# Optimization experiments

Hardware: AMD Instinct MI355X
Metric: run time of the kernel (lower is better)

Reference implementation:

```python
import jax, jax.numpy as jnp
import numpy as np

B, S, HID = 2, 2048, 2048
NH, NKV, D = 16, 4, 128  # heads, kv heads, dim_per_head
ROPE_BASE = 10000.0


def setup_inputs() -> dict:
    key = jax.random.key(0)
    ks = jax.random.split(key, 5)
    x = jax.random.normal(ks[0], (B, S, HID), jnp.float32)
    wq = jax.random.normal(ks[1], (HID, NH * D), jnp.float32) * 0.02
    wk = jax.random.normal(ks[2], (HID, NKV * D), jnp.float32) * 0.02
    wv = jax.random.normal(ks[3], (HID, NKV * D), jnp.float32) * 0.02
    wo = jax.random.normal(ks[4], (NH * D, HID), jnp.float32) * 0.02
    inv_freq = 1.0 / (ROPE_BASE ** (jnp.arange(0, D, 2, dtype=jnp.float32) / D))
    freqs = jnp.outer(jnp.arange(S, dtype=jnp.float32), inv_freq)  # [S, D/2]
    cos, sin = jnp.cos(freqs), jnp.sin(freqs)
    mask = jnp.tril(jnp.ones((S, S), dtype=bool))  # causal, True = attend
    return {"x": x, "wq": wq, "wk": wk, "wv": wv, "wo": wo,
            "cos": cos, "sin": sin, "mask": mask}


def _rope_interleave(t, cos, sin):
    # t: [B, H, S, D]; cos/sin: [S, D/2]; interleaved pairs (even, odd)
    te, to = t[..., ::2], t[..., 1::2]
    c, s = cos[None, None], sin[None, None]
    re = te * c - to * s
    ro = to * c + te * s
    return jnp.stack([re, ro], axis=-1).reshape(t.shape)


def reference(x, wq, wk, wv, wo, cos, sin, mask):
    b, s, _ = x.shape
    # QKV projections + shape(): [B, S, hid] -> [B, H, S, D]
    q = (x @ wq).reshape(b, s, NH, D).transpose(0, 2, 1, 3)
    k = (x @ wk).reshape(b, s, NKV, D).transpose(0, 2, 1, 3)
    v = (x @ wv).reshape(b, s, NKV, D).transpose(0, 2, 1, 3)
    q = _rope_interleave(q, cos, sin)
    k = _rope_interleave(k, cos, sin)
    # GQA: repeat each kv head heads//heads_kv times consecutively
    rep = NH // NKV
    k = jnp.repeat(k, rep, axis=1)
    v = jnp.repeat(v, rep, axis=1)
    scores = jnp.einsum('bhqd,bhkd->bhqk', q, k) * (D ** -0.5)
    scores = scores.astype(jnp.float32)
    scores = jnp.where(mask[None, None], scores, jnp.finfo(jnp.float32).min)
    attn = jax.nn.softmax(scores, axis=-1).astype(x.dtype)
    ctx = jnp.einsum('bhqk,bhkd->bhqd', attn, v)
    ctx = ctx.transpose(0, 2, 1, 3).reshape(b, s, NH * D)  # unshape()
    return ctx @ wo
```

## Files before the change

kernel.cpp:

```cpp
#include <hip/hip_runtime.h>
#include <hip/hip_bf16.h>
#include <math.h>

#define S_LEN 2048
#define HIDW 2048
#define NHEAD 16
#define NKVH 4
#define HD 128
#define NB 2
#define MROWS (NB * S_LEN)
#define QKVN (NHEAD * HD + 2 * NKVH * HD)
#define KOFF (NHEAD * HD)
#define VOFF (NHEAD * HD + NKVH * HD)

typedef __bf16 bf16_t;
typedef __bf16 bf16x4_t __attribute__((ext_vector_type(4)));
typedef __bf16 bf16x8_t __attribute__((ext_vector_type(8)));
typedef float f32x4_t __attribute__((ext_vector_type(4)));

__device__ __forceinline__ void gload_lds16(const bf16_t* g, bf16_t* l) {
  __builtin_amdgcn_global_load_lds(
      (const __attribute__((address_space(1))) void*)g,
      (__attribute__((address_space(3))) void*)l, 16, 0, 0);
}

__device__ __forceinline__ f32x4_t zero4() {
  f32x4_t z = {0.f, 0.f, 0.f, 0.f};
  return z;
}

__device__ __forceinline__ float fexp2(float x) {
#if __has_builtin(__builtin_amdgcn_exp2f)
  return __builtin_amdgcn_exp2f(x);
#else
  return exp2f(x);
#endif
}

__global__ __launch_bounds__(256) void k_cvt8(const float* __restrict__ in,
                                              bf16_t* __restrict__ out, int n8) {
  int i = blockIdx.x * 256 + threadIdx.x;
  if (i >= n8) return;
  const float4* p = (const float4*)(in + (size_t)i * 8);
  float4 a = p[0], b = p[1];
  bf16x8_t r;
  r[0] = (bf16_t)a.x; r[1] = (bf16_t)a.y; r[2] = (bf16_t)a.z; r[3] = (bf16_t)a.w;
  r[4] = (bf16_t)b.x; r[5] = (bf16_t)b.y; r[6] = (bf16_t)b.z; r[7] = (bf16_t)b.w;
  *(bf16x8_t*)(out + (size_t)i * 8) = r;
}

__global__ __launch_bounds__(256) void k_tr_cvt(const float* __restrict__ in,
                                                bf16_t* __restrict__ out, int R, int C) {
  __shared__ float t[32][33];
  int c0 = blockIdx.x * 32, r0 = blockIdx.y * 32;
  int tx = threadIdx.x & 31, ty = threadIdx.x >> 5;
#pragma unroll
  for (int rr = ty; rr < 32; rr += 8) t[rr][tx] = in[(size_t)(r0 + rr) * C + c0 + tx];
  __syncthreads();
#pragma unroll
  for (int rr = ty; rr < 32; rr += 8)
    out[(size_t)(c0 + rr) * R + r0 + tx] = (bf16_t)t[tx][rr];
}

template <int EPI, int BMH>
__global__ __launch_bounds__(512, 2) void k_gemm256(const bf16_t* __restrict__ A,
                                                    const bf16_t* __restrict__ Bt,
                                                    void* __restrict__ Cout,
                                                    int M, int N, int K, int nby,
                                                    const float* __restrict__ cosT,
                                                    const float* __restrict__ sinT) {
  __shared__ bf16_t As[2][BMH * 128 * 64];
  __shared__ bf16_t Bs[2][256 * 64];

  int tid = threadIdx.x;
  int lane = tid & 63, wid = tid >> 6;
  int l15 = lane & 15, lg = lane >> 4;
  int wrb = (wid >> 2) * (BMH * 64);
  int wcb = (wid & 3) * 64;

  int nwg = gridDim.x;
  int qx = nwg >> 3;
  int lin = blockIdx.x;
  int wg = (lin & 7) * qx + (lin >> 3);
  int row0 = (wg / nby) * (BMH * 128), col0 = (wg % nby) * 256;

  int srow = tid >> 3;
  int scol = ((tid & 7) ^ (srow & 7)) * 8;
  const bf16_t* Ag = A + (size_t)(row0 + srow) * K + scol;
  const bf16_t* Bg = Bt + (size_t)(col0 + srow) * K + scol;

  f32x4_t acc[BMH * 4][4];
#pragma unroll
  for (int i = 0; i < BMH * 4; i++)
#pragma unroll
    for (int j = 0; j < 4; j++) acc[i][j] = zero4();

  int xr = (l15 & 7) << 4;
  int nk = K >> 6;

  auto stA = [&](int tt, int u) {
    gload_lds16(Ag + (size_t)u * 64 * K + (size_t)tt * 64,
                As[tt & 1] + u * 4096 + tid * 8);
  };
  auto stB = [&](int tt, int u) {
    gload_lds16(Bg + (size_t)u * 64 * K + (size_t)tt * 64,
                Bs[tt & 1] + u * 4096 + tid * 8);
  };

  for (int tt = 0; tt < 2 && tt < nk; tt++) {
    for (int u = 0; u < BMH * 2; u++) stA(tt, u);
    for (int u = 0; u < 4; u++) stB(tt, u);
  }
  if (nk > 1) {
    if constexpr (BMH == 2) asm volatile("s_waitcnt vmcnt(8)" ::: "memory");
    else asm volatile("s_waitcnt vmcnt(6)" ::: "memory");
  } else {
    asm volatile("s_waitcnt vmcnt(0)" ::: "memory");
  }
  __builtin_amdgcn_s_barrier();
  __builtin_amdgcn_sched_barrier(0);

  for (int t = 0; t < nk; t++) {
    int cur = t & 1;
    const char* Ac = (const char*)As[cur];
    const char* Bc = (const char*)Bs[cur];
    bool pf = (t + 2 < nk);

    bf16x8_t af0[4][2], bfr[4][2];
#pragma unroll
    for (int i = 0; i < 4; i++) {
      int row = wrb + i * 16 + l15;
#pragma unroll
      for (int kk = 0; kk < 2; kk++)
        af0[i][kk] = *(const bf16x8_t*)(Ac + ((row * 128 + kk * 64 + lg * 16) ^ xr));
    }
#pragma unroll
    for (int jn = 0; jn < 4; jn++) {
      int rowb = wcb + jn * 16 + l15;
#pragma unroll
      for (int kk = 0; kk < 2; kk++)
        bfr[jn][kk] = *(const bf16x8_t*)(Bc + ((rowb * 128 + kk * 64 + lg * 16) ^ xr));
    }
    __builtin_amdgcn_s_barrier();
    __builtin_amdgcn_s_setprio(1);
    if constexpr (BMH == 2) {
#pragma unroll
      for (int i = 0; i < 4; i++)
#pragma unroll
        for (int j = 0; j < 2; j++)
#pragma unroll
          for (int kk = 0; kk < 2; kk++)
            acc[i][j] = __builtin_amdgcn_mfma_f32_16x16x32_bf16(af0[i][kk], bfr[j][kk],
                                                                acc[i][j], 0, 0, 0);
    } else {
#pragma unroll
      for (int i = 0; i < 4; i++)
#pragma unroll
        for (int kk = 0; kk < 2; kk++)
          acc[i][0] = __builtin_amdgcn_mfma_f32_16x16x32_bf16(af0[i][kk], bfr[0][kk],
                                                              acc[i][0], 0, 0, 0);
    }
    __builtin_amdgcn_s_setprio(0);

    if (pf) {
      stA(t + 2, 0);
      if constexpr (BMH == 2) stA(t + 2, 2);
      else stA(t + 2, 1);
    }
    __builtin_amdgcn_s_barrier();
    __builtin_amdgcn_s_setprio(1);
    if constexpr (BMH == 2) {
#pragma unroll
      for (int i = 0; i < 4; i++)
#pragma unroll
        for (int j = 0; j < 2; j++)
#pragma unroll
          for (int kk = 0; kk < 2; kk++)
            acc[i][2 + j] = __builtin_amdgcn_mfma_f32_16x16x32_bf16(
                af0[i][kk], bfr[2 + j][kk], acc[i][2 + j], 0, 0, 0);
    } else {
#pragma unroll
      for (int i = 0; i < 4; i++)
#pragma unroll
        for (int kk = 0; kk < 2; kk++)
          acc[i][1] = __builtin_amdgcn_mfma_f32_16x16x32_bf16(af0[i][kk], bfr[1][kk],
                                                              acc[i][1], 0, 0, 0);
    }
    __builtin_amdgcn_s_setprio(0);

    bf16x8_t af1[4][2];
    if constexpr (BMH == 2) {
#pragma unroll
      for (int i = 0; i < 4; i++) {
        int row = wrb + 64 + i * 16 + l15;
#pragma unroll
        for (int kk = 0; kk < 2; kk++)
          af1[i][kk] = *(const bf16x8_t*)(Ac + ((row * 128 + kk * 64 + lg * 16) ^ xr));
      }
    }
    if (pf) { stB(t + 2, 0); stB(t + 2, 1); }
    __builtin_amdgcn_s_barrier();
    __builtin_amdgcn_s_setprio(1);
    if constexpr (BMH == 2) {
#pragma unroll
      for (int i = 0; i < 4; i++)
#pragma unroll
        for (int j = 0; j < 2; j++)
#pragma unroll
          for (int kk = 0; kk < 2; kk++)
            acc[4 + i][j] = __builtin_amdgcn_mfma_f32_16x16x32_bf16(
                af1[i][kk], bfr[j][kk], acc[4 + i][j], 0, 0, 0);
    } else {
#pragma unroll
      for (int i = 0; i < 4; i++)
#pragma unroll
        for (int kk = 0; kk < 2; kk++)
          acc[i][2] = __builtin_amdgcn_mfma_f32_16x16x32_bf16(af0[i][kk], bfr[2][kk],
                                                              acc[i][2], 0, 0, 0);
    }
    __builtin_amdgcn_s_setprio(0);

    if (pf) {
      stB(t + 2, 2); stB(t + 2, 3);
      if constexpr (BMH == 2) { stA(t + 2, 1); stA(t + 2, 3); }
    }
    __builtin_amdgcn_s_barrier();
    __builtin_amdgcn_s_setprio(1);
    if constexpr (BMH == 2) {
#pragma unroll
      for (int i = 0; i < 4; i++)
#pragma unroll
        for (int j = 0; j < 2; j++)
#pragma unroll
          for (int kk = 0; kk < 2; kk++)
            acc[4 + i][2 + j] = __builtin_amdgcn_mfma_f32_16x16x32_bf16(
                af1[i][kk], bfr[2 + j][kk], acc[4 + i][2 + j], 0, 0, 0);
    } else {
#pragma unroll
      for (int i = 0; i < 4; i++)
#pragma unroll
        for (int kk = 0; kk < 2; kk++)
          acc[i][3] = __builtin_amdgcn_mfma_f32_16x16x32_bf16(af0[i][kk], bfr[3][kk],
                                                              acc[i][3], 0, 0, 0);
    }
    __builtin_amdgcn_s_setprio(0);

    if (t + 1 < nk) {
      if (pf) {
        if constexpr (BMH == 2) asm volatile("s_waitcnt vmcnt(8)" ::: "memory");
        else asm volatile("s_waitcnt vmcnt(6)" ::: "memory");
      } else {
        asm volatile("s_waitcnt vmcnt(0)" ::: "memory");
      }
    }
    __builtin_amdgcn_s_barrier();
    __builtin_amdgcn_sched_barrier(0);
  }

  if (EPI == 2) {
    if (col0 < VOFF) {
      int sbase = row0 & (S_LEN - 1);
      bf16_t* cosL = &As[0][0];
      bf16_t* sinL = &Bs[0][0];
#pragma unroll
      for (int k = 0; k < 8; k++) {
        gload_lds16((const bf16_t*)(cosT + (size_t)sbase * 64 + k * 2048 + tid * 4),
                    cosL + k * 4096 + tid * 8);
        gload_lds16((const bf16_t*)(sinT + (size_t)sbase * 64 + k * 2048 + tid * 4),
                    sinL + k * 4096 + tid * 8);
      }
      asm volatile("s_waitcnt vmcnt(0)" ::: "memory");
      __builtin_amdgcn_s_barrier();
      const float* cosF = (const float*)cosL;
      const float* sinF = (const float*)sinL;
      const float QS = 0.08838834764831845f * 1.4426950408889634f;
#pragma unroll
      for (int i = 0; i < BMH * 4; i++) {
#pragma unroll
        for (int j = 0; j < 4; j++) {
          int c = col0 + wcb + j * 16 + l15;
          int rlb = wrb + i * 16 + lg * 4;
          float scale = (c < KOFF) ? QS : 1.0f;
          int p0 = (c & 127) >> 1;
          int codd = c & 1;
#pragma unroll
          for (int qd = 0; qd < 4; qd++) {
            int rl = rlb + qd;
            float self = acc[i][j][qd];
            float other = __shfl_xor(self, 1);
            float cv = cosF[rl * 64 + p0], sv = sinF[rl * 64 + p0];
            float outv = codd ? (self * cv + other * sv) : (self * cv - other * sv);
            ((bf16_t*)Cout)[(size_t)(row0 + rl) * N + c] = (bf16_t)(outv * scale);
          }
        }
      }
    } else {
#pragma unroll
      for (int i = 0; i < BMH * 4; i++) {
#pragma unroll
        for (int j = 0; j < 4; j++) {
          int r = row0 + wrb + i * 16 + lg * 4;
          int c = col0 + wcb + j * 16 + l15;
#pragma unroll
          for (int qd = 0; qd < 4; qd++)
            ((bf16_t*)Cout)[(size_t)(r + qd) * N + c] = (bf16_t)acc[i][j][qd];
        }
      }
    }
  } else {
#pragma unroll
    for (int i = 0; i < BMH * 4; i++) {
#pragma unroll
      for (int j = 0; j < 4; j++) {
        int r = row0 + wrb + i * 16 + lg * 4;
        int c = col0 + wcb + j * 16 + l15;
#pragma unroll
        for (int qd = 0; qd < 4; qd++)
          ((float*)Cout)[(size_t)(r + qd) * N + c] = acc[i][j][qd];
      }
    }
  }
}

__global__ __launch_bounds__(256) void k_vt(const bf16_t* __restrict__ qkv,
                                            bf16_t* __restrict__ vt) {
  __shared__ bf16_t t[32][33];
  int s0 = blockIdx.x * 32;
  int dt = (blockIdx.y & 3) * 32;
  int h = blockIdx.y >> 2;
  int b = blockIdx.z;
  int tx = threadIdx.x & 31, ty = threadIdx.x >> 5;
#pragma unroll
  for (int rr = ty; rr < 32; rr += 8)
    t[rr][tx] = qkv[(size_t)(b * S_LEN + s0 + rr) * QKVN + VOFF + h * HD + dt + tx];
  __syncthreads();
#pragma unroll
  for (int rr = ty; rr < 32; rr += 8)
    vt[((size_t)((b * NKVH + h) * HD + dt + rr)) * S_LEN + s0 + tx] = t[tx][rr];
}

__global__ __launch_bounds__(256, 2) void k_attn(const bf16_t* __restrict__ qkv,
                                                 const bf16_t* __restrict__ vt,
                                                 bf16_t* __restrict__ ctx) {
  __shared__ bf16_t Ks[2 * 64 * 128];
  __shared__ bf16_t Vs[2 * 128 * 64];
  __shared__ bf16_t plds[4][16 * 72];

  int tid = threadIdx.x;
  int lane = tid & 63, wid = tid >> 6;
  int idx = blockIdx.x;
  int bh = idx & 31;
  int qg = 31 - (idx >> 5);
  int b = bh >> 4, h = bh & 15;
  int kvh = h >> 2;
  int q0 = qg * 64 + wid * 16;
  int l15 = lane & 15, lg = lane >> 4;

  const bf16_t* Kbase = qkv + (size_t)(b * S_LEN) * QKVN + KOFF + kvh * HD;
  const bf16_t* Vbase = vt + (size_t)(b * NKVH + kvh) * HD * S_LEN;

  const bf16_t* Qp = qkv + (size_t)(b * S_LEN + q0 + l15) * QKVN + h * HD + lg * 8;
  bf16x8_t aq[4];
#pragma unroll
  for (int kk = 0; kk < 4; kk++) aq[kk] = *(const bf16x8_t*)(Qp + kk * 32);

  int Ls[4], Lk[4], Lv[4];
#pragma unroll
  for (int u = 0; u < 4; u++) {
    int L = u * 4096 + tid * 16;
    Ls[u] = L >> 1;
    Lk[u] = L ^ (((L >> 8) & 7) << 4);
    Lv[u] = L ^ (((L >> 7) & 7) << 4);
  }

  f32x4_t o[8];
#pragma unroll
  for (int j = 0; j < 8; j++) o[j] = zero4();
  float ms = -INFINITY, lsum = 0.f;

  bf16_t* pbuf = &plds[wid][0];
  int xr = (l15 & 7) << 4;
  int ntiles = qg + 1;
  int qcol = q0 + l15;

#pragma unroll
  for (int u = 0; u < 4; u++) {
    gload_lds16(Kbase + (size_t)(Lk[u] >> 8) * QKVN + ((Lk[u] & 255) >> 1), Ks + Ls[u]);
    gload_lds16(Vbase + (size_t)(Lv[u] >> 7) * S_LEN + ((Lv[u] & 127) >> 1), Vs + Ls[u]);
  }
  __syncthreads();

  for (int t = 0; t < ntiles; t++) {
    int kv0 = t * 64;
    if (t + 1 < ntiles) {
      const bf16_t* Kn = Kbase + (size_t)(kv0 + 64) * QKVN;
      const bf16_t* Vn = Vbase + kv0 + 64;
      int bo = ((t + 1) & 1) * 8192;
#pragma unroll
      for (int u = 0; u < 4; u++) {
        gload_lds16(Kn + (size_t)(Lk[u] >> 8) * QKVN + ((Lk[u] & 255) >> 1), Ks + bo + Ls[u]);
        gload_lds16(Vn + (size_t)(Lv[u] >> 7) * S_LEN + ((Lv[u] & 127) >> 1), Vs + bo + Ls[u]);
      }
    }
    const char* Kb = (const char*)Ks + (t & 1) * 16384;
    const char* Vb = (const char*)Vs + (t & 1) * 16384;

    f32x4_t sacc[4];
#pragma unroll
    for (int cg = 0; cg < 4; cg++) sacc[cg] = zero4();
#pragma unroll
    for (int cg = 0; cg < 4; cg++) {
#pragma unroll
      for (int kk = 0; kk < 4; kk++) {
        int boff = ((cg * 16 + l15) * 256 + kk * 64 + lg * 16) ^ xr;
        bf16x8_t bk = *(const bf16x8_t*)(Kb + boff);
        sacc[cg] = __builtin_amdgcn_mfma_f32_16x16x32_bf16(bk, aq[kk], sacc[cg], 0, 0, 0);
      }
    }
    if (kv0 + 63 > q0) {
#pragma unroll
      for (int cg = 0; cg < 4; cg++) {
#pragma unroll
        for (int i = 0; i < 4; i++) {
          int kvg = kv0 + cg * 16 + lg * 4 + i;
          if (kvg > qcol) sacc[cg][i] = -1e30f;
        }
      }
    }
    float pmax = sacc[0][0];
#pragma unroll
    for (int cg = 0; cg < 4; cg++)
#pragma unroll
      for (int i = 0; i < 4; i++) pmax = fmaxf(pmax, sacc[cg][i]);
    pmax = fmaxf(pmax, __shfl_xor(pmax, 16));
    pmax = fmaxf(pmax, __shfl_xor(pmax, 32));
    if (__any(pmax - ms > 8.0f)) {
      float nm = fmaxf(ms, pmax);
      float sc = fexp2(ms - nm);
      ms = nm;
      lsum *= sc;
      float sci[4];
#pragma unroll
      for (int i = 0; i < 4; i++) sci[i] = __shfl(sc, lg * 4 + i);
#pragma unroll
      for (int j = 0; j < 8; j++)
#pragma unroll
        for (int i = 0; i < 4; i++) o[j][i] *= sci[i];
    }
    float ls = 0.f;
#pragma unroll
    for (int cg = 0; cg < 4; cg++)
#pragma unroll
      for (int i = 0; i < 4; i++) {
        sacc[cg][i] = fexp2(sacc[cg][i] - ms);
        ls += sacc[cg][i];
      }
    ls += __shfl_xor(ls, 16);
    ls += __shfl_xor(ls, 32);
    lsum += ls;
#pragma unroll
    for (int cg = 0; cg < 4; cg++)
#pragma unroll
      for (int i = 0; i < 4; i++)
        pbuf[l15 * 72 + cg * 16 + lg * 4 + i] = (bf16_t)sacc[cg][i];
    __builtin_amdgcn_wave_barrier();
    bf16x8_t pa0 = *(const bf16x8_t*)(pbuf + l15 * 72 + lg * 8);
    bf16x8_t pa1 = *(const bf16x8_t*)(pbuf + l15 * 72 + 32 + lg * 8);
    __builtin_amdgcn_wave_barrier();
#pragma unroll
    for (int j = 0; j < 8; j++) {
      int d = j * 16 + l15;
      int bo0 = (d * 128 + lg * 16) ^ xr;
      int bo1 = (d * 128 + 64 + lg * 16) ^ xr;
      o[j] = __builtin_amdgcn_mfma_f32_16x16x32_bf16(
          pa0, *(const bf16x8_t*)(Vb + bo0), o[j], 0, 0, 0);
      o[j] = __builtin_amdgcn_mfma_f32_16x16x32_bf16(
          pa1, *(const bf16x8_t*)(Vb + bo1), o[j], 0, 0, 0);
    }
    __syncthreads();
  }

  bf16_t* Cp = ctx + (size_t)(b * S_LEN + q0) * KOFF + h * HD;
#pragma unroll
  for (int i = 0; i < 4; i++) {
    float inv = 1.f / __shfl(lsum, lg * 4 + i);
    int row = lg * 4 + i;
#pragma unroll
    for (int j = 0; j < 8; j++)
      Cp[(size_t)row * KOFF + j * 16 + l15] = (bf16_t)(o[j][i] * inv);
  }
}

extern "C" void kernel_launch(void* const* d_in, const int* in_sizes, int n_in,
                              void* d_out, int out_size, void* d_ws, size_t ws_size,
                              hipStream_t stream) {
  const float* x = (const float*)d_in[0];
  const float* wq = (const float*)d_in[1];
  const float* wk = (const float*)d_in[2];
  const float* wv = (const float*)d_in[3];
  const float* wo = (const float*)d_in[4];
  const float* cosT = (const float*)d_in[5];
  const float* sinT = (const float*)d_in[6];

  bf16_t* xb = (bf16_t*)d_ws;
  bf16_t* wqkvT = xb + (size_t)MROWS * HIDW;
  bf16_t* woT = wqkvT + (size_t)QKVN * HIDW;
  bf16_t* qkv = woT + (size_t)HIDW * HIDW;
  bf16_t* vtb = qkv + (size_t)MROWS * QKVN;

  k_cvt8<<<MROWS * HIDW / 8 / 256, 256, 0, stream>>>(x, xb, MROWS * HIDW / 8);
  k_tr_cvt<<<dim3(KOFF / 32, HIDW / 32), 256, 0, stream>>>(wq, wqkvT, HIDW, KOFF);
  k_tr_cvt<<<dim3((NKVH * HD) / 32, HIDW / 32), 256, 0, stream>>>(
      wk, wqkvT + (size_t)KOFF * HIDW, HIDW, NKVH * HD);
  k_tr_cvt<<<dim3((NKVH * HD) / 32, HIDW / 32), 256, 0, stream>>>(
      wv, wqkvT + (size_t)VOFF * HIDW, HIDW, NKVH * HD);
  k_tr_cvt<<<dim3(HIDW / 32, KOFF / 32), 256, 0, stream>>>(wo, woT, KOFF, HIDW);
  k_gemm256<2, 2><<<(MROWS / 256) * (QKVN / 256), 512, 0, stream>>>(
      xb, wqkvT, qkv, MROWS, QKVN, HIDW, QKVN / 256, cosT, sinT);
  k_vt<<<dim3(S_LEN / 32, 4 * NKVH, NB), 256, 0, stream>>>(qkv, vtb);
  k_attn<<<32 * 32, 256, 0, stream>>>(qkv, vtb, xb);
  k_gemm256<0, 1><<<(MROWS / 128) * (HIDW / 256), 512, 0, stream>>>(
      xb, woT, d_out, MROWS, HIDW, KOFF, HIDW / 256, nullptr, nullptr);
}
```

Measured before the change: 193.9 us.

## Process two query sub-tiles per attention block to reuse K/V tiles

The attention kernel now handles 128 query rows per block, as two 64-row sub-tiles per wave, instead of 64. Each K/V tile loaded into LDS is used for both sub-tiles, which halves K/V global traffic per query, and the grid shrinks to 512 blocks. Blocks are paired so that blocks with many causal tiles and blocks with few are interleaved for load balance. In exchange, register pressure roughly doubles for the accumulators and Q fragments, which may lower occupancy under the 2-block launch bound, and there are fewer blocks to fill the machine.

```diff
diff --git a/kernel.cpp b/kernel.cpp
--- a/kernel.cpp
+++ b/kernel.cpp
@@ -14,7 +14,6 @@
 #define VOFF (NHEAD * HD + NKVH * HD)
 
 typedef __bf16 bf16_t;
-typedef __bf16 bf16x4_t __attribute__((ext_vector_type(4)));
 typedef __bf16 bf16x8_t __attribute__((ext_vector_type(8)));
 typedef float f32x4_t __attribute__((ext_vector_type(4)));
 
@@ -121,9 +120,8 @@
   __builtin_amdgcn_sched_barrier(0);
 
   for (int t = 0; t < nk; t++) {
-    int cur = t & 1;
-    const char* Ac = (const char*)As[cur];
-    const char* Bc = (const char*)Bs[cur];
+    const char* Ac = (const char*)As[t & 1];
+    const char* Bc = (const char*)Bs[t & 1];
     bool pf = (t + 2 < nk);
 
     bf16x8_t af0[4][2], bfr[4][2];
@@ -350,19 +348,23 @@
   int lane = tid & 63, wid = tid >> 6;
   int idx = blockIdx.x;
   int bh = idx & 31;
-  int qg = 31 - (idx >> 5);
+  int p = (idx >> 5) & 7;
+  int qg = (idx < 256) ? (15 - p) : p;
   int b = bh >> 4, h = bh & 15;
   int kvh = h >> 2;
-  int q0 = qg * 64 + wid * 16;
   int l15 = lane & 15, lg = lane >> 4;
+  int q0s[2] = {qg * 128 + wid * 16, qg * 128 + 64 + wid * 16};
 
   const bf16_t* Kbase = qkv + (size_t)(b * S_LEN) * QKVN + KOFF + kvh * HD;
   const bf16_t* Vbase = vt + (size_t)(b * NKVH + kvh) * HD * S_LEN;
 
-  const bf16_t* Qp = qkv + (size_t)(b * S_LEN + q0 + l15) * QKVN + h * HD + lg * 8;
-  bf16x8_t aq[4];
-#pragma unroll
-  for (int kk = 0; kk < 4; kk++) aq[kk] = *(const bf16x8_t*)(Qp + kk * 32);
+  bf16x8_t aq[2][4];
+#pragma unroll
+  for (int s = 0; s < 2; s++) {
+    const bf16_t* Qp = qkv + (size_t)(b * S_LEN + q0s[s] + l15) * QKVN + h * HD + lg * 8;
+#pragma unroll
+    for (int kk = 0; kk < 4; kk++) aq[s][kk] = *(const bf16x8_t*)(Qp + kk * 32);
+  }
 
   int Ls[4], Lk[4], Lv[4];
 #pragma unroll
@@ -373,15 +375,16 @@
     Lv[u] = L ^ (((L >> 7) & 7) << 4);
   }
 
-  f32x4_t o[8];
-#pragma unroll
-  for (int j = 0; j < 8; j++) o[j] = zero4();
-  float ms = -INFINITY, lsum = 0.f;
+  f32x4_t o[2][8];
+#pragma unroll
+  for (int s = 0; s < 2; s++)
+#pragma unroll
+    for (int j = 0; j < 8; j++) o[s][j] = zero4();
+  float ms[2] = {-INFINITY, -INFINITY}, lsum[2] = {0.f, 0.f};
 
   bf16_t* pbuf = &plds[wid][0];
   int xr = (l15 & 7) << 4;
-  int ntiles = qg + 1;
-  int qcol = q0 + l15;
+  int ntiles = 2 * qg + 2;
 
 #pragma unroll
   for (int u = 0; u < 4; u++) {
@@ -405,89 +408,99 @@
     const char* Kb = (const char*)Ks + (t & 1) * 16384;
     const char* Vb = (const char*)Vs + (t & 1) * 16384;
 
-    f32x4_t sacc[4];
-#pragma unroll
-    for (int cg = 0; cg < 4; cg++) sacc[cg] = zero4();
-#pragma unroll
-    for (int cg = 0; cg < 4; cg++) {
-#pragma unroll
-      for (int kk = 0; kk < 4; kk++) {
-        int boff = ((cg * 16 + l15) * 256 + kk * 64 + lg * 16) ^ xr;
-        bf16x8_t bk = *(const bf16x8_t*)(Kb + boff);
-        sacc[cg] = __builtin_amdgcn_mfma_f32_16x16x32_bf16(bk, aq[kk], sacc[cg], 0, 0, 0);
-      }
-    }
-    if (kv0 + 63 > q0) {
+#pragma unroll
+    for (int s = 0; s < 2; s++) {
+      int q0 = q0s[s];
+      if (kv0 > q0 + 15) continue;
+      int qcol = q0 + l15;
+
+      f32x4_t sacc[4];
+#pragma unroll
+      for (int cg = 0; cg < 4; cg++) sacc[cg] = zero4();
 #pragma unroll
       for (int cg = 0; cg < 4; cg++) {
 #pragma unroll
+        for (int kk = 0; kk < 4; kk++) {
+          int boff = ((cg * 16 + l15) * 256 + kk * 64 + lg * 16) ^ xr;
+          bf16x8_t bk = *(const bf16x8_t*)(Kb + boff);
+          sacc[cg] = __builtin_amdgcn_mfma_f32_16x16x32_bf16(bk, aq[s][kk], sacc[cg], 0, 0, 0);
+        }
+      }
+      if (kv0 + 63 > q0) {
+#pragma unroll
+        for (int cg = 0; cg < 4; cg++) {
+#pragma unroll
+          for (int i = 0; i < 4; i++) {
+            int kvg = kv0 + cg * 16 + lg * 4 + i;
+            if (kvg > qcol) sacc[cg][i] = -1e30f;
+          }
+        }
+      }
+      float pmax = sacc[0][0];
+#pragma unroll
+      for (int cg = 0; cg < 4; cg++)
+#pragma unroll
+        for (int i = 0; i < 4; i++) pmax = fmaxf(pmax, sacc[cg][i]);
+      pmax = fmaxf(pmax, __shfl_xor(pmax, 16));
+      pmax = fmaxf(pmax, __shfl_xor(pmax, 32));
+      if (__any(pmax - ms[s] > 8.0f)) {
+        float nm = fmaxf(ms[s], pmax);
+        float sc = fexp2(ms[s] - nm);
+        ms[s] = nm;
+        lsum[s] *= sc;
+        float sci[4];
+#pragma unroll
+        for (int i = 0; i < 4; i++) sci[i] = __shfl(sc, lg * 4 + i);
+#pragma unroll
+        for (int j = 0; j < 8; j++)
+#pragma unroll
+          for (int i = 0; i < 4; i++) o[s][j][i] *= sci[i];
+      }
+      float ls = 0.f;
+#pragma unroll
+      for (int cg = 0; cg < 4; cg++)
+#pragma unroll
         for (int i = 0; i < 4; i++) {
-          int kvg = kv0 + cg * 16 + lg * 4 + i;
-          if (kvg > qcol) sacc[cg][i] = -1e30f;
+          sacc[cg][i] = fexp2(sacc[cg][i] - ms[s]);
+          ls += sacc[cg][i];
         }
-      }
-    }
-    float pmax = sacc[0][0];
-#pragma unroll
-    for (int cg = 0; cg < 4; cg++)
-#pragma unroll
-      for (int i = 0; i < 4; i++) pmax = fmaxf(pmax, sacc[cg][i]);
-    pmax = fmaxf(pmax, __shfl_xor(pmax, 16));
-    pmax = fmaxf(pmax, __shfl_xor(pmax, 32));
-    if (__any(pmax - ms > 8.0f)) {
-      float nm = fmaxf(ms, pmax);
-      float sc = fexp2(ms - nm);
-      ms = nm;
-      lsum *= sc;
-      float sci[4];
-#pragma unroll
-      for (int i = 0; i < 4; i++) sci[i] = __shfl(sc, lg * 4 + i);
+      ls += __shfl_xor(ls, 16);
+      ls += __shfl_xor(ls, 32);
+      lsum[s] += ls;
+#pragma unroll
+      for (int cg = 0; cg < 4; cg++)
+#pragma unroll
+        for (int i = 0; i < 4; i++)
+          pbuf[l15 * 72 + cg * 16 + lg * 4 + i] = (bf16_t)sacc[cg][i];
+      __builtin_amdgcn_wave_barrier();
+      bf16x8_t pa0 = *(const bf16x8_t*)(pbuf + l15 * 72 + lg * 8);
+      bf16x8_t pa1 = *(const bf16x8_t*)(pbuf + l15 * 72 + 32 + lg * 8);
+      __builtin_amdgcn_wave_barrier();
+#pragma unroll
+      for (int j = 0; j < 8; j++) {
+        int d = j * 16 + l15;
+        int bo0 = (d * 128 + lg * 16) ^ xr;
+        int bo1 = (d * 128 + 64 + lg * 16) ^ xr;
+        o[s][j] = __builtin_amdgcn_mfma_f32_16x16x32_bf16(
+            pa0, *(const bf16x8_t*)(Vb + bo0), o[s][j], 0, 0, 0);
+        o[s][j] = __builtin_amdgcn_mfma_f32_16x16x32_bf16(
+            pa1, *(const bf16x8_t*)(Vb + bo1), o[s][j], 0, 0, 0);
+      }
+    }
+    __syncthreads();
+  }
+
+#pragma unroll
+  for (int s = 0; s < 2; s++) {
+    bf16_t* Cp = ctx + (size_t)(b * S_LEN + q0s[s]) * KOFF + h * HD;
+#pragma unroll
+    for (int i = 0; i < 4; i++) {
+      float inv = 1.f / __shfl(lsum[s], lg * 4 + i);
+      int row = lg * 4 + i;
 #pragma unroll
       for (int j = 0; j < 8; j++)
-#pragma unroll
-        for (int i = 0; i < 4; i++) o[j][i] *= sci[i];
-    }
-    float ls = 0.f;
-#pragma unroll
-    for (int cg = 0; cg < 4; cg++)
-#pragma unroll
-      for (int i = 0; i < 4; i++) {
-        sacc[cg][i] = fexp2(sacc[cg][i] - ms);
-        ls += sacc[cg][i];
-      }
-    ls += __shfl_xor(ls, 16);
-    ls += __shfl_xor(ls, 32);
-    lsum += ls;
-#pragma unroll
-    for (int cg = 0; cg < 4; cg++)
-#pragma unroll
-      for (int i = 0; i < 4; i++)
-        pbuf[l15 * 72 + cg * 16 + lg * 4 + i] = (bf16_t)sacc[cg][i];
-    __builtin_amdgcn_wave_barrier();
-    bf16x8_t pa0 = *(const bf16x8_t*)(pbuf + l15 * 72 + lg * 8);
-    bf16x8_t pa1 = *(const bf16x8_t*)(pbuf + l15 * 72 + 32 + lg * 8);
-    __builtin_amdgcn_wave_barrier();
-#pragma unroll
-    for (int j = 0; j < 8; j++) {
-      int d = j * 16 + l15;
-      int bo0 = (d * 128 + lg * 16) ^ xr;
-      int bo1 = (d * 128 + 64 + lg * 16) ^ xr;
-      o[j] = __builtin_amdgcn_mfma_f32_16x16x32_bf16(
-          pa0, *(const bf16x8_t*)(Vb + bo0), o[j], 0, 0, 0);
-      o[j] = __builtin_amdgcn_mfma_f32_16x16x32_bf16(
-          pa1, *(const bf16x8_t*)(Vb + bo1), o[j], 0, 0, 0);
-    }
-    __syncthreads();
-  }
-
-  bf16_t* Cp = ctx + (size_t)(b * S_LEN + q0) * KOFF + h * HD;
-#pragma unroll
-  for (int i = 0; i < 4; i++) {
-    float inv = 1.f / __shfl(lsum, lg * 4 + i);
-    int row = lg * 4 + i;
-#pragma unroll
-    for (int j = 0; j < 8; j++)
-      Cp[(size_t)row * KOFF + j * 16 + l15] = (bf16_t)(o[j][i] * inv);
+        Cp[(size_t)row * KOFF + j * 16 + l15] = (bf16_t)(o[s][j][i] * inv);
+    }
   }
 }
 
@@ -518,7 +531,7 @@
   k_gemm256<2, 2><<<(MROWS / 256) * (QKVN / 256), 512, 0, stream>>>(
       xb, wqkvT, qkv, MROWS, QKVN, HIDW, QKVN / 256, cosT, sinT);
   k_vt<<<dim3(S_LEN / 32, 4 * NKVH, NB), 256, 0, stream>>>(qkv, vtb);
-  k_attn<<<32 * 32, 256, 0, stream>>>(qkv, vtb, xb);
+  k_attn<<<32 * 16, 256, 0, stream>>>(qkv, vtb, xb);
   k_gemm256<0, 1><<<(MROWS / 128) * (HIDW / 256), 512, 0, stream>>>(
       xb, woT, d_out, MROWS, HIDW, KOFF, HIDW / 256, nullptr, nullptr);
 }
```

New measurement: 214.2 us. +10.5%, slower.
